# Kernel tuning notes

Measured on AMD Instinct MI355X. Metric: run time of the kernel, lower is better.

## Reference

```python
import jax, jax.numpy as jnp
import numpy as np

B, N, D = 64, 128, 32
P = N * (N - 1)          # ordered pairs
H1, H2, HF = 32, 32, 16  # layer_widths=(32,32), final_widths=(16,)
EPS = 1e-5
SLOPE = 0.01             # LeakyReLU default


def _leaky(x):
    return jnp.where(x >= 0, x, SLOPE * x)


def setup_inputs() -> dict:
    key = jax.random.key(0)
    ks = jax.random.split(key, 16)
    # all ordered pairs (i, j), i != j, grouped by source i
    src = np.repeat(np.arange(N), N - 1)
    tgt = np.array([j for i in range(N) for j in range(N) if j != i])
    s = 0.1
    return {
        "inputs": jax.random.normal(ks[0], (B, N, D), jnp.float32),
        "src": jnp.asarray(src, jnp.int32),
        "tgt": jnp.asarray(tgt, jnp.int32),
        # edge MLP: Linear(2D,32) -> BN1d(P) -> LeakyReLU -> Linear(32,32) -> LeakyReLU -> Linear(32, 1+D)
        "W1": jax.random.normal(ks[1], (2 * D, H1), jnp.float32) * s,
        "b1": jnp.zeros((H1,), jnp.float32),
        "g1": jnp.ones((P,), jnp.float32),
        "be1": jnp.zeros((P,), jnp.float32),
        "W2": jax.random.normal(ks[2], (H1, H2), jnp.float32) * s,
        "b2": jnp.zeros((H2,), jnp.float32),
        "W3": jax.random.normal(ks[3], (H2, 1 + D), jnp.float32) * s,
        "b3": jnp.zeros((1 + D,), jnp.float32),
        # final MLP: Linear(2D,16) -> BN1d(16) -> LeakyReLU -> Linear(16, D)
        "Wf1": jax.random.normal(ks[4], (2 * D, HF), jnp.float32) * s,
        "bf1": jnp.zeros((HF,), jnp.float32),
        "gf": jnp.ones((HF,), jnp.float32),
        "bef": jnp.zeros((HF,), jnp.float32),
        "Wf2": jax.random.normal(ks[5], (HF, D), jnp.float32) * s,
        "bf2": jnp.zeros((D,), jnp.float32),
    }


def reference(inputs, src, tgt, W1, b1, g1, be1, W2, b2, W3, b3,
              Wf1, bf1, gf, bef, Wf2, bf2):
    b, n, d = inputs.shape
    # gather pair features: (B, P, 2D)
    paired = jnp.concatenate([inputs[:, src], inputs[:, tgt]], axis=2)
    h = paired @ W1 + b1                              # (B, P, H1)
    # BatchNorm1d(P) on (B, P, H1): normalize per pair channel over (batch, feat)
    m = h.mean(axis=(0, 2), keepdims=True)
    v = h.var(axis=(0, 2), keepdims=True)
    h = (h - m) * jax.lax.rsqrt(v + EPS) * g1[None, :, None] + be1[None, :, None]
    h = _leaky(h) @ W2 + b2
    h = _leaky(h) @ W3 + b3                           # (B, P, 1+D)
    edges = jax.nn.sigmoid(h[..., :1])                # (B, P, 1)
    messages = h[..., 1:]                             # (B, P, D)
    weighted = edges * messages
    # segment-sum over the (N-1) senders per source node
    agg = weighted.reshape(b, n, n - 1, d).sum(axis=2)  # (B, N, D)
    sm = jnp.concatenate([inputs, agg], axis=2).reshape(-1, 2 * d)
    f = sm @ Wf1 + bf1                                # (B*N, HF)
    mf = f.mean(axis=0)
    vf = f.var(axis=0)
    f = (f - mf) * jax.lax.rsqrt(vf + EPS) * gf + bef
    out = _leaky(f) @ Wf2 + bf2
    return edges[..., 0], out.reshape(b, n, d)
```

## Files before the change

### kernel.cpp

```cpp
#include <hip/hip_runtime.h>
#include <hip/hip_bf16.h>
#include <math.h>

#define BB 64
#define NN 128
#define DD 32
#define PP (NN * (NN - 1))
#define EPSF 1e-5f

typedef __attribute__((ext_vector_type(8))) short bf16x8;
typedef __attribute__((ext_vector_type(4))) float f32x4;

static __device__ __forceinline__ unsigned short f2bf(float x) {
    unsigned u = __builtin_bit_cast(unsigned, x);
    u += 0x7fff + ((u >> 16) & 1);
    return (unsigned short)(u >> 16);
}
static __device__ __forceinline__ unsigned pk2bf(float a, float b) {
    float2 t; t.x = a; t.y = b;
    __hip_bfloat162 h = __float22bfloat162_rn(t);
    unsigned u;
    __builtin_memcpy(&u, &h, 4);
    return u;
}
static __device__ __forceinline__ float leakyf(float x) {
    return fmaxf(x, 0.01f * x);
}

__global__ __launch_bounds__(256) void proj_kernel(
    const float* __restrict__ inputs, const float* __restrict__ W1,
    const float* __restrict__ b1,
    const float* __restrict__ W2, const float* __restrict__ W3,
    float* __restrict__ AT, float* __restrict__ BT,
    unsigned short* __restrict__ ATh, unsigned short* __restrict__ BTh,
    float* __restrict__ SQp,
    unsigned short* __restrict__ W2p, unsigned short* __restrict__ W3p,
    float* __restrict__ fpartA, float* __restrict__ fpartB)
{
    __shared__ float Xs[16 * 33];
    __shared__ float W1s[2048];
    __shared__ float red[16];

    int tid = threadIdx.x;
    int n = blockIdx.x >> 2, q = blockIdx.x & 3;

    for (int idx = tid; idx < 2048; idx += 256) W1s[idx] = W1[idx];
    for (int idx = tid; idx < 512; idx += 256) {
        int r = idx >> 5, d = idx & 31;
        Xs[r * 33 + d] = inputs[(size_t)(q * 16 + r) * 4096 + n * 32 + d];
    }
    __syncthreads();

    int j = tid & 31, rb = tid >> 5;
    int lane = tid & 63, w = tid >> 6;
    float b1j = b1[j];
    float sa = 0.f, qa = 0.f, sb = 0.f, qb = 0.f;
    #pragma unroll
    for (int i = 0; i < 2; ++i) {
        int r = rb * 2 + i;
        int b = q * 16 + r;
        float a = b1j, c = 0.f;
        #pragma unroll
        for (int k = 0; k < 32; ++k) {
            float x = Xs[r * 33 + k];
            a += x * W1s[k * 32 + j];
            c += x * W1s[(32 + k) * 32 + j];
        }
        size_t off = ((size_t)n * 64 + b) * 32 + j;
        AT[off] = a;  BT[off] = c;
        ATh[off] = f2bf(a);  BTh[off] = f2bf(c);
        sa += a; qa += a * a; sb += c; qb += c * c;
    }
    #pragma unroll
    for (int d = 32; d > 0; d >>= 1) {
        sa += __shfl_down(sa, d, 64);
        qa += __shfl_down(qa, d, 64);
        sb += __shfl_down(sb, d, 64);
        qb += __shfl_down(qb, d, 64);
    }
    if (lane == 0) { red[w*4+0] = sa; red[w*4+1] = qa; red[w*4+2] = sb; red[w*4+3] = qb; }
    __syncthreads();
    if (tid == 0) {
        float4 v;
        v.x = red[0] + red[4] + red[8]  + red[12];
        v.y = red[1] + red[5] + red[9]  + red[13];
        v.z = red[2] + red[6] + red[10] + red[14];
        v.w = red[3] + red[7] + red[11] + red[15];
        ((float4*)SQp)[n * 4 + q] = v;
    }

    if (blockIdx.x == 0 && tid < 64) {
        int l = tid, nn2 = l & 15, kc = l >> 4;
        #pragma unroll
        for (int ct = 0; ct < 2; ++ct)
            #pragma unroll
            for (int jj = 0; jj < 8; ++jj) {
                int k = kc * 8 + jj;
                W2p[(ct * 64 + l) * 8 + jj] = f2bf(W2[k * 32 + ct * 16 + nn2]);
            }
        #pragma unroll
        for (int ct = 0; ct < 3; ++ct)
            #pragma unroll
            for (int jj = 0; jj < 8; ++jj) {
                int k = kc * 8 + jj;
                int c2 = ct * 16 + nn2;
                W3p[(ct * 64 + l) * 8 + jj] = f2bf(c2 < 33 ? W3[k * 33 + c2] : 0.f);
            }
    }
    if (blockIdx.x == 1) {
        for (int idx = tid; idx < 1024; idx += 256) {
            fpartA[idx] = 0.f;
            fpartB[idx] = 0.f;
        }
    }
}

__global__ __launch_bounds__(256) void stats2_kernel(
    const unsigned short* __restrict__ ATh, const unsigned short* __restrict__ BTh,
    const float* __restrict__ SQp,
    const float* __restrict__ g1, const float* __restrict__ be1,
    float* __restrict__ statA, float* __restrict__ statB)
{
    __shared__ __align__(16) float part[4 * 64 * 4];
    int tid = threadIdx.x;
    int lane = tid & 63, w = tid >> 6;
    int s0 = (blockIdx.x >> 3) * 16, t0 = (blockIdx.x & 7) * 16;

    int m = lane & 15, kc = lane >> 4;
    const unsigned short* abase = ATh + (size_t)(s0 + m) * 2048 + kc * 8 + w * 512;
    const unsigned short* bbase = BTh + (size_t)(t0 + m) * 2048 + kc * 8 + w * 512;

    f32x4 acc0 = {0.f, 0.f, 0.f, 0.f}, acc1 = {0.f, 0.f, 0.f, 0.f};
    #pragma unroll
    for (int step = 0; step < 8; ++step) {
        bf16x8 av0 = *(const bf16x8*)(abase + (2 * step) * 32);
        bf16x8 bv0 = *(const bf16x8*)(bbase + (2 * step) * 32);
        acc0 = __builtin_amdgcn_mfma_f32_16x16x32_bf16(av0, bv0, acc0, 0, 0, 0);
        bf16x8 av1 = *(const bf16x8*)(abase + (2 * step + 1) * 32);
        bf16x8 bv1 = *(const bf16x8*)(bbase + (2 * step + 1) * 32);
        acc1 = __builtin_amdgcn_mfma_f32_16x16x32_bf16(av1, bv1, acc1, 0, 0, 0);
    }
    f32x4 acc;
    acc[0] = acc0[0] + acc1[0]; acc[1] = acc0[1] + acc1[1];
    acc[2] = acc0[2] + acc1[2]; acc[3] = acc0[3] + acc1[3];
    *(f32x4*)&part[(w * 64 + lane) * 4] = acc;
    __syncthreads();

    if (w == 0) {
        #pragma unroll
        for (int ww = 1; ww < 4; ++ww) {
            f32x4 o2 = *(const f32x4*)&part[(ww * 64 + lane) * 4];
            acc[0] += o2[0]; acc[1] += o2[1]; acc[2] += o2[2]; acc[3] += o2[3];
        }
        int col = lane & 15, quad = lane >> 4;
        int t = t0 + col;
        float sbt = 0.f, qbt = 0.f;
        #pragma unroll
        for (int o2 = 0; o2 < 4; ++o2) {
            float4 v = ((const float4*)SQp)[t * 4 + o2];
            sbt += v.z; qbt += v.w;
        }
        #pragma unroll
        for (int r = 0; r < 4; ++r) {
            int s = s0 + quad * 4 + r;
            if (s != t) {
                float sas = 0.f, qas = 0.f;
                #pragma unroll
                for (int o2 = 0; o2 < 4; ++o2) {
                    float4 v = ((const float4*)SQp)[s * 4 + o2];
                    sas += v.x; qas += v.y;
                }
                int e = t - (t > s);
                int p = s * 127 + e;
                float S = sas + sbt;
                float Q = qas + qbt + 2.f * acc[r];
                float mean = S * (1.f / 2048.f);
                float var  = Q * (1.f / 2048.f) - mean * mean;
                float inv  = rsqrtf(var + EPSF);
                float sc   = inv * g1[p];
                statA[p] = sc;
                statB[p] = be1[p] - mean * sc;
            }
        }
    }
}

__global__ __launch_bounds__(256) void edges_kernel(
    const float* __restrict__ AT, const float* __restrict__ BT,
    const float* __restrict__ statA, const float* __restrict__ statB,
    const unsigned short* __restrict__ W2p, const unsigned short* __restrict__ W3p,
    const float* __restrict__ b2, const float* __restrict__ b3,
    const float* __restrict__ inputs, const float* __restrict__ Wf1,
    const float* __restrict__ bf1,
    float* __restrict__ edges_out,
    float* __restrict__ f, float* __restrict__ fpartA, float* __restrict__ fpartB)
{
    __shared__ __align__(16) unsigned short Hs[4][512];
    __shared__ float Wf1s[1024];
    __shared__ float aggbuf[4][32];

    int tid = threadIdx.x;
    int s = blockIdx.x & 127;
    int b = blockIdx.x >> 7;
    int lane = tid & 63, w = tid >> 6;
    int m = lane & 15;
    int kb = lane >> 4;
    int col = m;
    int q4 = kb * 4;
    int qbase = lane & 48;

    for (int idx = tid; idx < 1024; idx += 256) Wf1s[idx] = Wf1[idx];

    bf16x8 wb2[2], wb3[3];
    wb2[0] = *(const bf16x8*)(W2p + (0 * 64 + lane) * 8);
    wb2[1] = *(const bf16x8*)(W2p + (1 * 64 + lane) * 8);
    wb3[0] = *(const bf16x8*)(W3p + (0 * 64 + lane) * 8);
    wb3[1] = *(const bf16x8*)(W3p + (1 * 64 + lane) * 8);
    wb3[2] = *(const bf16x8*)(W3p + (2 * 64 + lane) * 8);
    float b2c0 = b2[col], b2c1 = b2[16 + col];
    float b3c[3];
    #pragma unroll
    for (int ct = 0; ct < 3; ++ct) {
        int c = ct * 16 + col;
        b3c[ct] = (c < 33) ? b3[c] : 0.f;
    }

    const float4* asl = (const float4*)(AT + ((size_t)s * 64 + b) * 32 + kb * 8);
    float4 a0 = asl[0], a1 = asl[1];

    float aggpart[3] = {0.f, 0.f, 0.f};

    #pragma unroll
    for (int rt = 0; rt < 2; ++rt) {
        int tile = w * 2 + rt;
        int e = tile * 16 + m;
        bool valid = (e < 127);
        int ee = valid ? e : 0;
        int t = ee + (ee >= s);
        int p = s * 127 + ee;
        float sc = statA[p], sh = statB[p];

        const float4* bsl = (const float4*)(BT + ((size_t)t * 64 + b) * 32 + kb * 8);
        float4 bv0 = bsl[0], bv1 = bsl[1];

        float nh[8];
        nh[0] = leakyf((a0.x + bv0.x) * sc + sh);
        nh[1] = leakyf((a0.y + bv0.y) * sc + sh);
        nh[2] = leakyf((a0.z + bv0.z) * sc + sh);
        nh[3] = leakyf((a0.w + bv0.w) * sc + sh);
        nh[4] = leakyf((a1.x + bv1.x) * sc + sh);
        nh[5] = leakyf((a1.y + bv1.y) * sc + sh);
        nh[6] = leakyf((a1.z + bv1.z) * sc + sh);
        nh[7] = leakyf((a1.w + bv1.w) * sc + sh);
        if (!valid) {
            #pragma unroll
            for (int q = 0; q < 8; ++q) nh[q] = 0.f;
        }
        union { bf16x8 v; unsigned u[4]; } AF;
        #pragma unroll
        for (int q = 0; q < 4; ++q) AF.u[q] = pk2bf(nh[2*q], nh[2*q+1]);

        f32x4 c0 = {0.f, 0.f, 0.f, 0.f}, c1 = {0.f, 0.f, 0.f, 0.f};
        c0 = __builtin_amdgcn_mfma_f32_16x16x32_bf16(AF.v, wb2[0], c0, 0, 0, 0);
        c1 = __builtin_amdgcn_mfma_f32_16x16x32_bf16(AF.v, wb2[1], c1, 0, 0, 0);

        #pragma unroll
        for (int reg = 0; reg < 4; ++reg) {
            int row = q4 + reg;
            float x = leakyf(c0[reg] + b2c0);
            float y = leakyf(c1[reg] + b2c1);
            int cA = col;
            int cB = col + 16;
            Hs[w][row * 32 + (((cA >> 3) ^ (row >> 2)) & 3) * 8 + (cA & 7)] = f2bf(x);
            Hs[w][row * 32 + (((cB >> 3) ^ (row >> 2)) & 3) * 8 + (cB & 7)] = f2bf(y);
        }
        bf16x8 a2 = *(const bf16x8*)&Hs[w][m * 32 + ((kb ^ (m >> 2)) & 3) * 8];

        f32x4 oo[3];
        #pragma unroll
        for (int ct = 0; ct < 3; ++ct) {
            f32x4 cc = {0.f, 0.f, 0.f, 0.f};
            oo[ct] = __builtin_amdgcn_mfma_f32_16x16x32_bf16(a2, wb3[ct], cc, 0, 0, 0);
        }

        float v0 = 0.f, v1 = 0.f, v2 = 0.f, v3 = 0.f;
        int grow0 = tile * 16 + q4;
        if (col == 0) {
            v0 = 1.f / (1.f + __expf(-(oo[0][0] + b3c[0])));
            v1 = 1.f / (1.f + __expf(-(oo[0][1] + b3c[0])));
            v2 = 1.f / (1.f + __expf(-(oo[0][2] + b3c[0])));
            v3 = (grow0 == 124) ? 0.f
               : 1.f / (1.f + __expf(-(oo[0][3] + b3c[0])));
            float* ep = edges_out + (size_t)b * PP + s * 127 + grow0;
            ep[0] = v0; ep[1] = v1; ep[2] = v2;
            if (grow0 != 124) ep[3] = v3;
        }
        float ev0 = __shfl(v0, qbase, 64);
        float ev1 = __shfl(v1, qbase, 64);
        float ev2 = __shfl(v2, qbase, 64);
        float ev3 = __shfl(v3, qbase, 64);

        #pragma unroll
        for (int ct = 0; ct < 3; ++ct) {
            float bb3 = b3c[ct];
            float pt = ev0 * (oo[ct][0] + bb3) + ev1 * (oo[ct][1] + bb3)
                     + ev2 * (oo[ct][2] + bb3) + ev3 * (oo[ct][3] + bb3);
            aggpart[ct] += pt;
        }
    }

    #pragma unroll
    for (int ct = 0; ct < 3; ++ct) {
        float pt = aggpart[ct];
        pt += __shfl_xor(pt, 16, 64);
        pt += __shfl_xor(pt, 32, 64);
        int c = ct * 16 + col;
        if (kb == 0 && c >= 1 && c <= 32) aggbuf[w][c - 1] = pt;
    }
    __syncthreads();

    if (tid < 16) {
        size_t row = (size_t)b * 128 + s;
        const float* xrow = inputs + row * 32;
        float acc = bf1[tid];
        #pragma unroll
        for (int k = 0; k < 32; ++k) acc += xrow[k] * Wf1s[k * 16 + tid];
        #pragma unroll
        for (int k = 0; k < 32; ++k) {
            float tot = aggbuf[0][k] + aggbuf[1][k] + aggbuf[2][k] + aggbuf[3][k];
            acc += tot * Wf1s[(32 + k) * 16 + tid];
        }
        f[row * 16 + tid] = acc;
        int bucket = blockIdx.x & 63;
        atomicAdd(&fpartA[bucket * 16 + tid], acc);
        atomicAdd(&fpartB[bucket * 16 + tid], acc * acc);
    }
}

__global__ __launch_bounds__(256) void out_kernel(
    const float* __restrict__ f,
    const float* __restrict__ fpartA, const float* __restrict__ fpartB,
    const float* __restrict__ gf, const float* __restrict__ bef,
    const float* __restrict__ Wf2, const float* __restrict__ bf2,
    float* __restrict__ outp)
{
    __shared__ float Wf2s[512];
    __shared__ float sc[16], sh[16];
    __shared__ float fs[128];

    int tid = threadIdx.x;
    for (int idx = tid; idx < 512; idx += 256) Wf2s[idx] = Wf2[idx];
    if (tid < 16) {
        float S = 0.f, Q = 0.f;
        #pragma unroll
        for (int g = 0; g < 64; ++g) {
            S += fpartA[g * 16 + tid];
            Q += fpartB[g * 16 + tid];
        }
        float mean = S * (1.f / 8192.f);
        float var  = Q * (1.f / 8192.f) - mean * mean;
        float inv  = rsqrtf(var + EPSF);
        float s2   = inv * gf[tid];
        sc[tid] = s2;
        sh[tid] = bef[tid] - mean * s2;
    }
    int row0 = blockIdx.x * 8;
    if (tid < 128) {
        int r = tid >> 4, j = tid & 15;
        fs[r * 16 + j] = f[(size_t)(row0 + r) * 16 + j];
    }
    __syncthreads();

    int rl = tid >> 5, d = tid & 31;
    float acc = bf2[d];
    #pragma unroll
    for (int j = 0; j < 16; ++j) {
        float v = fs[rl * 16 + j] * sc[j] + sh[j];
        v = leakyf(v);
        acc += v * Wf2s[j * 32 + d];
    }
    outp[(size_t)(row0 + rl) * 32 + d] = acc;
}

extern "C" void kernel_launch(void* const* d_in, const int* in_sizes, int n_in,
                              void* d_out, int out_size, void* d_ws, size_t ws_size,
                              hipStream_t stream) {
    const float* inputs = (const float*)d_in[0];
    const float* W1   = (const float*)d_in[3];
    const float* b1   = (const float*)d_in[4];
    const float* g1   = (const float*)d_in[5];
    const float* be1  = (const float*)d_in[6];
    const float* W2   = (const float*)d_in[7];
    const float* b2   = (const float*)d_in[8];
    const float* W3   = (const float*)d_in[9];
    const float* b3   = (const float*)d_in[10];
    const float* Wf1  = (const float*)d_in[11];
    const float* bf1  = (const float*)d_in[12];
    const float* gf   = (const float*)d_in[13];
    const float* bef  = (const float*)d_in[14];
    const float* Wf2  = (const float*)d_in[15];
    const float* bf2  = (const float*)d_in[16];

    float* ws = (float*)d_ws;
    float* AT     = ws;
    float* BT     = ws + 262144;
    unsigned short* ATh = (unsigned short*)(ws + 524288);
    unsigned short* BTh = ATh + 262144;
    float* SQp    = ws + 786432;
    float* statA  = ws + 790528;
    float* statB  = ws + 806784;
    float* f      = ws + 823040;
    float* fpartA = ws + 954112;
    float* fpartB = ws + 955136;
    unsigned short* W2p = (unsigned short*)(ws + 956160);
    unsigned short* W3p = W2p + 1024;

    float* edges_out = (float*)d_out;
    float* outp      = edges_out + (size_t)BB * PP;

    proj_kernel<<<512, 256, 0, stream>>>(inputs, W1, b1, W2, W3,
                                         AT, BT, ATh, BTh, SQp,
                                         W2p, W3p, fpartA, fpartB);
    stats2_kernel<<<64, 256, 0, stream>>>(ATh, BTh, SQp, g1, be1, statA, statB);
    edges_kernel<<<8192, 256, 0, stream>>>(AT, BT, statA, statB, W2p, W3p,
                                           b2, b3, inputs, Wf1, bf1,
                                           edges_out, f, fpartA, fpartB);
    out_kernel<<<1024, 256, 0, stream>>>(f, fpartA, fpartB, gf, bef, Wf2, bf2, outp);
}
```

Measured before the change: 142.7 us.

## Process two batches per edges block and interleave BN scale/shift stats

Each edges_kernel block now handles two batch indices for the same source node, halving the grid. The per-pair BN scale/shift, the W2/W3 fragments, the Wf1 shared-memory copy and the bias loads are then reused across both batches instead of being reloaded per block. statA/statB are merged into one interleaved float2 array so each lane does a single 8-byte load. The cost is more registers per thread and fewer blocks to hide latency.

Result: slower. 145.8 us (+2.2%).

```diff
diff --git a/kernel.cpp b/kernel.cpp
--- a/kernel.cpp
+++ b/kernel.cpp
@@ -119,7 +119,7 @@
     const unsigned short* __restrict__ ATh, const unsigned short* __restrict__ BTh,
     const float* __restrict__ SQp,
     const float* __restrict__ g1, const float* __restrict__ be1,
-    float* __restrict__ statA, float* __restrict__ statB)
+    float* __restrict__ statAB)
 {
     __shared__ __align__(16) float part[4 * 64 * 4];
     int tid = threadIdx.x;
@@ -178,8 +178,10 @@
                 float var  = Q * (1.f / 2048.f) - mean * mean;
                 float inv  = rsqrtf(var + EPSF);
                 float sc   = inv * g1[p];
-                statA[p] = sc;
-                statB[p] = be1[p] - mean * sc;
+                float2 st;
+                st.x = sc;
+                st.y = be1[p] - mean * sc;
+                ((float2*)statAB)[p] = st;
             }
         }
     }
@@ -187,7 +189,7 @@
 
 __global__ __launch_bounds__(256) void edges_kernel(
     const float* __restrict__ AT, const float* __restrict__ BT,
-    const float* __restrict__ statA, const float* __restrict__ statB,
+    const float* __restrict__ statAB,
     const unsigned short* __restrict__ W2p, const unsigned short* __restrict__ W3p,
     const float* __restrict__ b2, const float* __restrict__ b3,
     const float* __restrict__ inputs, const float* __restrict__ Wf1,
@@ -197,11 +199,11 @@
 {
     __shared__ __align__(16) unsigned short Hs[4][512];
     __shared__ float Wf1s[1024];
-    __shared__ float aggbuf[4][32];
+    __shared__ float aggbuf[2][4][32];
 
     int tid = threadIdx.x;
     int s = blockIdx.x & 127;
-    int b = blockIdx.x >> 7;
+    int b0 = (blockIdx.x >> 7) * 2;
     int lane = tid & 63, w = tid >> 6;
     int m = lane & 15;
     int kb = lane >> 4;
@@ -225,115 +227,131 @@
         b3c[ct] = (c < 33) ? b3[c] : 0.f;
     }
 
-    const float4* asl = (const float4*)(AT + ((size_t)s * 64 + b) * 32 + kb * 8);
-    float4 a0 = asl[0], a1 = asl[1];
-
-    float aggpart[3] = {0.f, 0.f, 0.f};
-
+    int tr[2];
+    float sc_[2], sh_[2];
+    bool valid_[2];
+    int grow_[2];
     #pragma unroll
     for (int rt = 0; rt < 2; ++rt) {
         int tile = w * 2 + rt;
         int e = tile * 16 + m;
         bool valid = (e < 127);
         int ee = valid ? e : 0;
-        int t = ee + (ee >= s);
-        int p = s * 127 + ee;
-        float sc = statA[p], sh = statB[p];
-
-        const float4* bsl = (const float4*)(BT + ((size_t)t * 64 + b) * 32 + kb * 8);
-        float4 bv0 = bsl[0], bv1 = bsl[1];
-
-        float nh[8];
-        nh[0] = leakyf((a0.x + bv0.x) * sc + sh);
-        nh[1] = leakyf((a0.y + bv0.y) * sc + sh);
-        nh[2] = leakyf((a0.z + bv0.z) * sc + sh);
-        nh[3] = leakyf((a0.w + bv0.w) * sc + sh);
-        nh[4] = leakyf((a1.x + bv1.x) * sc + sh);
-        nh[5] = leakyf((a1.y + bv1.y) * sc + sh);
-        nh[6] = leakyf((a1.z + bv1.z) * sc + sh);
-        nh[7] = leakyf((a1.w + bv1.w) * sc + sh);
-        if (!valid) {
-            #pragma unroll
-            for (int q = 0; q < 8; ++q) nh[q] = 0.f;
-        }
-        union { bf16x8 v; unsigned u[4]; } AF;
-        #pragma unroll
-        for (int q = 0; q < 4; ++q) AF.u[q] = pk2bf(nh[2*q], nh[2*q+1]);
-
-        f32x4 c0 = {0.f, 0.f, 0.f, 0.f}, c1 = {0.f, 0.f, 0.f, 0.f};
-        c0 = __builtin_amdgcn_mfma_f32_16x16x32_bf16(AF.v, wb2[0], c0, 0, 0, 0);
-        c1 = __builtin_amdgcn_mfma_f32_16x16x32_bf16(AF.v, wb2[1], c1, 0, 0, 0);
-
-        #pragma unroll
-        for (int reg = 0; reg < 4; ++reg) {
-            int row = q4 + reg;
-            float x = leakyf(c0[reg] + b2c0);
-            float y = leakyf(c1[reg] + b2c1);
-            int cA = col;
-            int cB = col + 16;
-            Hs[w][row * 32 + (((cA >> 3) ^ (row >> 2)) & 3) * 8 + (cA & 7)] = f2bf(x);
-            Hs[w][row * 32 + (((cB >> 3) ^ (row >> 2)) & 3) * 8 + (cB & 7)] = f2bf(y);
-        }
-        bf16x8 a2 = *(const bf16x8*)&Hs[w][m * 32 + ((kb ^ (m >> 2)) & 3) * 8];
-
-        f32x4 oo[3];
+        tr[rt] = ee + (ee >= s);
+        valid_[rt] = valid;
+        grow_[rt] = tile * 16 + q4;
+        float2 st = ((const float2*)statAB)[s * 127 + ee];
+        sc_[rt] = st.x; sh_[rt] = st.y;
+    }
+
+    float aggpart[2][3] = {{0.f,0.f,0.f},{0.f,0.f,0.f}};
+
+    #pragma unroll
+    for (int bsel = 0; bsel < 2; ++bsel) {
+        int b = b0 + bsel;
+        const float4* asl = (const float4*)(AT + ((size_t)s * 64 + b) * 32 + kb * 8);
+        float4 a0 = asl[0], a1 = asl[1];
+
+        #pragma unroll
+        for (int rt = 0; rt < 2; ++rt) {
+            float sc = sc_[rt], sh = sh_[rt];
+            const float4* bsl = (const float4*)(BT + ((size_t)tr[rt] * 64 + b) * 32 + kb * 8);
+            float4 bv0 = bsl[0], bv1 = bsl[1];
+
+            float nh[8];
+            nh[0] = leakyf((a0.x + bv0.x) * sc + sh);
+            nh[1] = leakyf((a0.y + bv0.y) * sc + sh);
+            nh[2] = leakyf((a0.z + bv0.z) * sc + sh);
+            nh[3] = leakyf((a0.w + bv0.w) * sc + sh);
+            nh[4] = leakyf((a1.x + bv1.x) * sc + sh);
+            nh[5] = leakyf((a1.y + bv1.y) * sc + sh);
+            nh[6] = leakyf((a1.z + bv1.z) * sc + sh);
+            nh[7] = leakyf((a1.w + bv1.w) * sc + sh);
+            if (!valid_[rt]) {
+                #pragma unroll
+                for (int q = 0; q < 8; ++q) nh[q] = 0.f;
+            }
+            union { bf16x8 v; unsigned u[4]; } AF;
+            #pragma unroll
+            for (int q = 0; q < 4; ++q) AF.u[q] = pk2bf(nh[2*q], nh[2*q+1]);
+
+            f32x4 c0 = {0.f, 0.f, 0.f, 0.f}, c1 = {0.f, 0.f, 0.f, 0.f};
+            c0 = __builtin_amdgcn_mfma_f32_16x16x32_bf16(AF.v, wb2[0], c0, 0, 0, 0);
+            c1 = __builtin_amdgcn_mfma_f32_16x16x32_bf16(AF.v, wb2[1], c1, 0, 0, 0);
+
+            #pragma unroll
+            for (int reg = 0; reg < 4; ++reg) {
+                int row = q4 + reg;
+                float x = leakyf(c0[reg] + b2c0);
+                float y = leakyf(c1[reg] + b2c1);
+                int cA = col;
+                int cB = col + 16;
+                Hs[w][row * 32 + (((cA >> 3) ^ (row >> 2)) & 3) * 8 + (cA & 7)] = f2bf(x);
+                Hs[w][row * 32 + (((cB >> 3) ^ (row >> 2)) & 3) * 8 + (cB & 7)] = f2bf(y);
+            }
+            bf16x8 a2 = *(const bf16x8*)&Hs[w][m * 32 + ((kb ^ (m >> 2)) & 3) * 8];
+
+            f32x4 oo[3];
+            #pragma unroll
+            for (int ct = 0; ct < 3; ++ct) {
+                f32x4 cc = {0.f, 0.f, 0.f, 0.f};
+                oo[ct] = __builtin_amdgcn_mfma_f32_16x16x32_bf16(a2, wb3[ct], cc, 0, 0, 0);
+            }
+
+            float v0 = 0.f, v1 = 0.f, v2 = 0.f, v3 = 0.f;
+            int grow0 = grow_[rt];
+            if (col == 0) {
+                v0 = 1.f / (1.f + __expf(-(oo[0][0] + b3c[0])));
+                v1 = 1.f / (1.f + __expf(-(oo[0][1] + b3c[0])));
+                v2 = 1.f / (1.f + __expf(-(oo[0][2] + b3c[0])));
+                v3 = (grow0 == 124) ? 0.f
+                   : 1.f / (1.f + __expf(-(oo[0][3] + b3c[0])));
+                float* ep = edges_out + (size_t)b * PP + s * 127 + grow0;
+                ep[0] = v0; ep[1] = v1; ep[2] = v2;
+                if (grow0 != 124) ep[3] = v3;
+            }
+            float ev0 = __shfl(v0, qbase, 64);
+            float ev1 = __shfl(v1, qbase, 64);
+            float ev2 = __shfl(v2, qbase, 64);
+            float ev3 = __shfl(v3, qbase, 64);
+
+            #pragma unroll
+            for (int ct = 0; ct < 3; ++ct) {
+                float bb3 = b3c[ct];
+                float pt = ev0 * (oo[ct][0] + bb3) + ev1 * (oo[ct][1] + bb3)
+                         + ev2 * (oo[ct][2] + bb3) + ev3 * (oo[ct][3] + bb3);
+                aggpart[bsel][ct] += pt;
+            }
+        }
+
         #pragma unroll
         for (int ct = 0; ct < 3; ++ct) {
-            f32x4 cc = {0.f, 0.f, 0.f, 0.f};
-            oo[ct] = __builtin_amdgcn_mfma_f32_16x16x32_bf16(a2, wb3[ct], cc, 0, 0, 0);
-        }
-
-        float v0 = 0.f, v1 = 0.f, v2 = 0.f, v3 = 0.f;
-        int grow0 = tile * 16 + q4;
-        if (col == 0) {
-            v0 = 1.f / (1.f + __expf(-(oo[0][0] + b3c[0])));
-            v1 = 1.f / (1.f + __expf(-(oo[0][1] + b3c[0])));
-            v2 = 1.f / (1.f + __expf(-(oo[0][2] + b3c[0])));
-            v3 = (grow0 == 124) ? 0.f
-               : 1.f / (1.f + __expf(-(oo[0][3] + b3c[0])));
-            float* ep = edges_out + (size_t)b * PP + s * 127 + grow0;
-            ep[0] = v0; ep[1] = v1; ep[2] = v2;
-            if (grow0 != 124) ep[3] = v3;
-        }
-        float ev0 = __shfl(v0, qbase, 64);
-        float ev1 = __shfl(v1, qbase, 64);
-        float ev2 = __shfl(v2, qbase, 64);
-        float ev3 = __shfl(v3, qbase, 64);
-
-        #pragma unroll
-        for (int ct = 0; ct < 3; ++ct) {
-            float bb3 = b3c[ct];
-            float pt = ev0 * (oo[ct][0] + bb3) + ev1 * (oo[ct][1] + bb3)
-                     + ev2 * (oo[ct][2] + bb3) + ev3 * (oo[ct][3] + bb3);
-            aggpart[ct] += pt;
-        }
-    }
-
-    #pragma unroll
-    for (int ct = 0; ct < 3; ++ct) {
-        float pt = aggpart[ct];
-        pt += __shfl_xor(pt, 16, 64);
-        pt += __shfl_xor(pt, 32, 64);
-        int c = ct * 16 + col;
-        if (kb == 0 && c >= 1 && c <= 32) aggbuf[w][c - 1] = pt;
+            float pt = aggpart[bsel][ct];
+            pt += __shfl_xor(pt, 16, 64);
+            pt += __shfl_xor(pt, 32, 64);
+            int c = ct * 16 + col;
+            if (kb == 0 && c >= 1 && c <= 32) aggbuf[bsel][w][c - 1] = pt;
+        }
     }
     __syncthreads();
 
-    if (tid < 16) {
-        size_t row = (size_t)b * 128 + s;
+    if (tid < 32) {
+        int bsel = tid >> 4, j = tid & 15;
+        size_t row = (size_t)(b0 + bsel) * 128 + s;
         const float* xrow = inputs + row * 32;
-        float acc = bf1[tid];
-        #pragma unroll
-        for (int k = 0; k < 32; ++k) acc += xrow[k] * Wf1s[k * 16 + tid];
+        float acc = bf1[j];
+        #pragma unroll
+        for (int k = 0; k < 32; ++k) acc += xrow[k] * Wf1s[k * 16 + j];
         #pragma unroll
         for (int k = 0; k < 32; ++k) {
-            float tot = aggbuf[0][k] + aggbuf[1][k] + aggbuf[2][k] + aggbuf[3][k];
-            acc += tot * Wf1s[(32 + k) * 16 + tid];
-        }
-        f[row * 16 + tid] = acc;
-        int bucket = blockIdx.x & 63;
-        atomicAdd(&fpartA[bucket * 16 + tid], acc);
-        atomicAdd(&fpartB[bucket * 16 + tid], acc * acc);
+            float tot = aggbuf[bsel][0][k] + aggbuf[bsel][1][k]
+                      + aggbuf[bsel][2][k] + aggbuf[bsel][3][k];
+            acc += tot * Wf1s[(32 + k) * 16 + j];
+        }
+        f[row * 16 + j] = acc;
+        int bucket = ((blockIdx.x << 1) + bsel) & 63;
+        atomicAdd(&fpartA[bucket * 16 + j], acc);
+        atomicAdd(&fpartB[bucket * 16 + j], acc * acc);
     }
 }
 
@@ -407,8 +425,7 @@
     unsigned short* ATh = (unsigned short*)(ws + 524288);
     unsigned short* BTh = ATh + 262144;
     float* SQp    = ws + 786432;
-    float* statA  = ws + 790528;
-    float* statB  = ws + 806784;
+    float* statAB = ws + 790528;
     float* f      = ws + 823040;
     float* fpartA = ws + 954112;
     float* fpartB = ws + 955136;
@@ -421,8 +438,8 @@
     proj_kernel<<<512, 256, 0, stream>>>(inputs, W1, b1, W2, W3,
                                          AT, BT, ATh, BTh, SQp,
                                          W2p, W3p, fpartA, fpartB);
-    stats2_kernel<<<64, 256, 0, stream>>>(ATh, BTh, SQp, g1, be1, statA, statB);
-    edges_kernel<<<8192, 256, 0, stream>>>(AT, BT, statA, statB, W2p, W3p,
+    stats2_kernel<<<64, 256, 0, stream>>>(ATh, BTh, SQp, g1, be1, statAB);
+    edges_kernel<<<4096, 256, 0, stream>>>(AT, BT, statAB, W2p, W3p,
                                            b2, b3, inputs, Wf1, bf1,
                                            edges_out, f, fpartA, fpartB);
     out_kernel<<<1024, 256, 0, stream>>>(f, fpartA, fpartB, gf, bef, Wf2, bf2, outp);
```
